# Optimization experiments

Measured on AMD Instinct MI355X. Metric: run time of the kernel, lower is better.

The kernel has to match this reference:

```python
import jax, jax.numpy as jnp
import numpy as np
from jax import lax

E, H, TOPK = 32, 512, 4
B, S = 2, 1024

def setup_inputs() -> dict:
    key = jax.random.key(0)
    ks = jax.random.split(key, 5)
    scale = 0.05
    return {
        "x": jax.random.normal(ks[0], (B, S, H), dtype=jnp.float32),
        "gate_w": jax.random.normal(ks[1], (E, H), dtype=jnp.float32) * scale,
        "w_gate": jax.random.normal(ks[2], (E, 2 * H, H), dtype=jnp.float32) * scale,
        "w_up": jax.random.normal(ks[3], (E, 2 * H, H), dtype=jnp.float32) * scale,
        "w_down": jax.random.normal(ks[4], (E, H, 2 * H), dtype=jnp.float32) * scale,
        "top_k": TOPK,
    }

def reference(x, gate_w, w_gate, w_up, w_down, top_k):
    b, s, h = x.shape
    n = b * s
    e = gate_w.shape[0]
    xf = x.reshape(n, h)                                   # [N,H]
    logits = xf @ gate_w.T                                 # [N,E]
    probs = jax.nn.softmax(logits, axis=-1)
    w, sel = lax.top_k(probs, top_k)                       # [N,K]
    w = w / jnp.sum(w, axis=-1, keepdims=True)
    # per-(token,expert) combine weight; zero for unselected experts
    comb = jnp.zeros((n, e), dtype=x.dtype).at[
        jnp.arange(n)[:, None], sel].add(w)                # [N,E]

    def body(acc, ws):
        wg, wu, wd, ce = ws                                # [2H,H],[2H,H],[H,2H],[N]
        hidden = jax.nn.silu(xf @ wg.T) * (xf @ wu.T)      # [N,2H]
        out = hidden @ wd.T                                # [N,H]
        return acc + out * ce[:, None], None

    acc0 = jnp.zeros_like(xf)
    acc, _ = lax.scan(body, acc0, (w_gate, w_up, w_down, comb.T))
    return acc.reshape(b, s, h)
```

## Files before the change

### kernel.cpp

```cpp
#include <hip/hip_runtime.h>
#include <hip/hip_bf16.h>
#include <math.h>

#define NE 32
#define H 512
#define H2 1024
#define NTOK 2048
#define CAP 2048
#define BM 64
#define MAXT64 160
#define TSTRIDE 144

typedef __attribute__((ext_vector_type(8))) short bf16x8;
typedef __attribute__((ext_vector_type(4))) float f32x4;
typedef unsigned int uint;
typedef unsigned short ushort;

__device__ __forceinline__ uint bf16r(float f) {
    uint u = __float_as_uint(f);
    return (u + 0x7FFFu + ((u >> 16) & 1u)) >> 16;
}
__device__ __forceinline__ uint pack_bf16(float a, float b) {
    return bf16r(a) | (bf16r(b) << 16);
}
__device__ __forceinline__ float bf16f(ushort u) {
    return __uint_as_float(((uint)u) << 16);
}

__device__ __forceinline__ void dma16(const void* g, void* l) {
    __builtin_amdgcn_global_load_lds(
        (const __attribute__((address_space(1))) uint*)g,
        (__attribute__((address_space(3))) uint*)l, 16, 0, 0);
}

__global__ __launch_bounds__(256) void prep_kernel(
    const float* __restrict__ x, const float* __restrict__ gate_w,
    int* __restrict__ cnt, int* __restrict__ listTok, int* __restrict__ listPair,
    float* __restrict__ listW, ushort* __restrict__ xbf,
    const float* __restrict__ wg, const float* __restrict__ wu,
    const float* __restrict__ wd,
    ushort* __restrict__ wgb, ushort* __restrict__ wub, ushort* __restrict__ wdb)
{
    const int b = blockIdx.x;
    if (b >= 512) {
        const int b2 = b - 512;
        const float* src = (b2 < 8192) ? wg : (b2 < 16384) ? wu : wd;
        ushort*     dst  = (b2 < 8192) ? wgb : (b2 < 16384) ? wub : wdb;
        const size_t base = (size_t)(b2 & 8191) * 2048 + (size_t)threadIdx.x * 8;
        const float4* s = (const float4*)(src + base);
        float4 x0 = s[0], x1 = s[1];
        uint4 v;
        v.x = pack_bf16(x0.x, x0.y); v.y = pack_bf16(x0.z, x0.w);
        v.z = pack_bf16(x1.x, x1.y); v.w = pack_bf16(x1.z, x1.w);
        *(uint4*)(dst + base) = v;
        return;
    }

    const int wave = threadIdx.x >> 6;
    const int lane = threadIdx.x & 63;
    const int t = b * 4 + wave;
    const int e = lane & 31;
    const int half = lane >> 5;

    const float4* xr = (const float4*)(x + (size_t)t * H + half * 256);
    const float4* gr = (const float4*)(gate_w + (size_t)e * H + half * 256);
    float acc = 0.f;
#pragma unroll 8
    for (int i = 0; i < 64; ++i) {
        float4 a = xr[i], g = gr[i];
        acc += a.x * g.x + a.y * g.y + a.z * g.z + a.w * g.w;
    }
    acc += __shfl_xor(acc, 32);

    float mx = acc;
#pragma unroll
    for (int m = 16; m >= 1; m >>= 1) mx = fmaxf(mx, __shfl_xor(mx, m));
    float p = __expf(acc - mx);
    float s = p;
#pragma unroll
    for (int m = 16; m >= 1; m >>= 1) s += __shfl_xor(s, m);
    float prob = p / s;

    int selk[4]; float wk[4]; float sum4 = 0.f;
#pragma unroll
    for (int k = 0; k < 4; ++k) {
        float v = prob; int idx = e;
#pragma unroll
        for (int m = 16; m >= 1; m >>= 1) {
            float v2 = __shfl_xor(v, m);
            int   i2 = __shfl_xor(idx, m);
            if (v2 > v || (v2 == v && i2 < idx)) { v = v2; idx = i2; }
        }
        selk[k] = idx; wk[k] = v; sum4 += v;
        if (e == idx) prob = -1.f;
    }

    if (lane == 0) {
#pragma unroll
        for (int k = 0; k < 4; ++k) {
            int ex = selk[k];
            int pos = atomicAdd(&cnt[ex], 1);
            listTok [ex * CAP + pos] = t;
            listPair[ex * CAP + pos] = t * 4 + k;
            listW   [ex * CAP + pos] = wk[k] / sum4;
        }
    }

    const float4* xrow4 = (const float4*)(x + (size_t)t * H);
    float4 a0 = xrow4[lane * 2];
    float4 a1 = xrow4[lane * 2 + 1];
    uint4 o;
    o.x = pack_bf16(a0.x, a0.y); o.y = pack_bf16(a0.z, a0.w);
    o.z = pack_bf16(a1.x, a1.y); o.w = pack_bf16(a1.z, a1.w);
    ((uint4*)(xbf + (size_t)t * H))[lane] = o;
}

__global__ void sched_kernel(const int* __restrict__ cnt,
                             int* __restrict__ ntiles, int* __restrict__ desc)
{
    const int lane = threadIdx.x;
    int t = 0;
    if (lane < NE) t = (cnt[lane] + 63) >> 6;
    int pre = t;
#pragma unroll
    for (int m = 1; m < 64; m <<= 1) {
        int v = __shfl_up(pre, m);
        if (lane >= m) pre += v;
    }
    const int off = pre - t;
    if (lane < NE)
        for (int i = 0; i < t; ++i) desc[off + i] = (lane << 16) | i;
    if (lane == 63) *ntiles = pre;
}

template<bool WB>
__global__ __launch_bounds__(256, 4) void moe_gemm1(
    const void* __restrict__ wgate_, const void* __restrict__ wup_,
    const ushort* __restrict__ xbf, const int* __restrict__ cnt,
    const int* __restrict__ listTok, const int* __restrict__ listPair,
    const float* __restrict__ listW, ushort* __restrict__ hidden,
    const int* __restrict__ ntiles, const int* __restrict__ desc)
{
    const int item = blockIdx.x;
    if (item >= (*ntiles) * 8) return;
    const int d  = desc[item >> 3];
    const int ch = item & 7;
    const int e  = d >> 16;
    const int mt = d & 0xffff;
    const int count = cnt[e];
    const int m0 = mt * BM;

    __shared__ ushort smem[2 * 128 * 64];
    ushort* Gs = smem;
    ushort* Us = smem + 128 * 64;

    const int tid  = threadIdx.x;
    const int lane = tid & 63;
    const int w    = tid >> 6;
    const int l15  = lane & 15;
    const int quad = lane >> 4;

    const int arow = m0 + w * 16 + l15;
    const int atok = (arow < count) ? listTok[e * CAP + arow] : 0;
    const char* aptr = (const char*)(xbf + (size_t)atok * H);

    const int rr = lane >> 3;
    const int p  = lane & 7;
    const char* gsrc = nullptr; const char* usrc = nullptr;
    const int sr = tid >> 1;
    const int sh = tid & 1;
    const float* gF = nullptr; const float* uF = nullptr;
    if (WB) {
        const ushort* wgp = (const ushort*)wgate_;
        const ushort* wup = (const ushort*)wup_;
        const size_t rowi = (size_t)e * H2 + (size_t)(ch * 128 + w * 32 + rr);
        gsrc = (const char*)(wgp + rowi * H) + ((p ^ rr) << 4);
        usrc = (const char*)(wup + rowi * H) + ((p ^ rr) << 4);
    } else {
        gF = (const float*)wgate_ + ((size_t)e * H2 + (size_t)(ch * 128 + sr)) * H;
        uF = (const float*)wup_   + ((size_t)e * H2 + (size_t)(ch * 128 + sr)) * H;
    }

    f32x4 accg[8], accu[8];
    const f32x4 fz = {0.f, 0.f, 0.f, 0.f};
#pragma unroll
    for (int ni = 0; ni < 8; ++ni) { accg[ni] = fz; accu[ni] = fz; }

    uint4 a0 = *(const uint4*)(aptr + quad * 16);
    uint4 a1 = *(const uint4*)(aptr + 64 + quad * 16);

    for (int it = 0; it < 8; ++it) {
        __syncthreads();
        if (WB) {
#pragma unroll
            for (int i = 0; i < 4; ++i) {
                dma16(gsrc + i * (8 * H * 2), (char*)Gs + w * 4096 + i * 1024);
                dma16(usrc + i * (8 * H * 2), (char*)Us + w * 4096 + i * 1024);
            }
        } else {
#pragma unroll
            for (int i = 0; i < 4; ++i) {
                const int pslot = sh * 4 + i;
                const int pc = pslot ^ (sr & 7);
                const float4* s1 = (const float4*)(gF + it * 64 + pc * 8);
                float4 g0 = s1[0], g1 = s1[1];
                uint4 v;
                v.x = pack_bf16(g0.x, g0.y); v.y = pack_bf16(g0.z, g0.w);
                v.z = pack_bf16(g1.x, g1.y); v.w = pack_bf16(g1.z, g1.w);
                ((uint4*)Gs)[sr * 8 + pslot] = v;
                const float4* s2 = (const float4*)(uF + it * 64 + pc * 8);
                float4 u0 = s2[0], u1 = s2[1];
                uint4 q;
                q.x = pack_bf16(u0.x, u0.y); q.y = pack_bf16(u0.z, u0.w);
                q.z = pack_bf16(u1.x, u1.y); q.w = pack_bf16(u1.z, u1.w);
                ((uint4*)Us)[sr * 8 + pslot] = q;
            }
        }
        const int itn = (it < 7) ? it + 1 : 7;
        uint4 an0 = *(const uint4*)(aptr + itn * 128 + quad * 16);
        uint4 an1 = *(const uint4*)(aptr + itn * 128 + 64 + quad * 16);
        __syncthreads();

#pragma unroll
        for (int ks = 0; ks < 2; ++ks) {
            bf16x8 af = ks ? *(bf16x8*)&a1 : *(bf16x8*)&a0;
#pragma unroll
            for (int ni = 0; ni < 8; ++ni) {
                const int n = ni * 16 + l15;
                const int slot = n * 8 + ((ks * 4 + quad) ^ (n & 7));
                bf16x8 bg = ((const bf16x8*)Gs)[slot];
                bf16x8 bu = ((const bf16x8*)Us)[slot];
                accg[ni] = __builtin_amdgcn_mfma_f32_16x16x32_bf16(af, bg, accg[ni], 0, 0, 0);
                accu[ni] = __builtin_amdgcn_mfma_f32_16x16x32_bf16(af, bu, accu[ni], 0, 0, 0);
            }
        }
        a0 = an0; a1 = an1;
        if (WB) { gsrc += 128; usrc += 128; }
    }

    __syncthreads();
    ushort* T = smem;
#pragma unroll
    for (int r = 0; r < 4; ++r) {
        const int row = w * 16 + quad * 4 + r;
        const int slot2 = m0 + row;
        const float wgt = (slot2 < count) ? listW[e * CAP + slot2] : 0.f;
#pragma unroll
        for (int ni = 0; ni < 8; ++ni) {
            float gv = accg[ni][r], uv = accu[ni][r];
            float hv = (gv / (1.f + __expf(-gv))) * uv * wgt;
            T[row * TSTRIDE + ni * 16 + l15] = (ushort)bf16r(hv);
        }
    }
    __syncthreads();
    {
        const int row = tid >> 2;
        const int qp  = tid & 3;
        const int slot2 = m0 + row;
        if (slot2 < count) {
            const int pr = listPair[e * CAP + slot2];
            uint4* dst = (uint4*)(hidden + (size_t)pr * H2 + ch * 128) + qp * 4;
            const uint4* src = (const uint4*)(T + row * TSTRIDE) + qp * 4;
#pragma unroll
            for (int i = 0; i < 4; ++i) dst[i] = src[i];
        }
    }
}

template<bool WB>
__global__ __launch_bounds__(256, 4) void moe_gemm2(
    const void* __restrict__ wdown_, const ushort* __restrict__ hidden,
    const int* __restrict__ cnt, const int* __restrict__ listPair,
    ushort* __restrict__ pairOut,
    const int* __restrict__ ntiles, const int* __restrict__ desc)
{
    const int item = blockIdx.x;
    if (item >= (*ntiles) * 8) return;
    const int d   = desc[item >> 3];
    const int ks2 = (item >> 2) & 1;
    const int ch  = item & 3;
    const int e   = d >> 16;
    const int mt  = d & 0xffff;
    const int count = cnt[e];
    const int m0 = mt * BM;

    __shared__ ushort smem[9216];
    ushort* Bs = smem;

    const int tid  = threadIdx.x;
    const int lane = tid & 63;
    const int w    = tid >> 6;
    const int l15  = lane & 15;
    const int quad = lane >> 4;

    const int arow = m0 + w * 16 + l15;
    const int apr  = (arow < count) ? listPair[e * CAP + arow] : 0;
    const char* aptr = (const char*)(hidden + (size_t)apr * H2 + ks2 * 512);

    const int rr = lane >> 3;
    const int p  = lane & 7;
    const char* bsrc = nullptr;
    const int sr = tid >> 1;
    const int sh = tid & 1;
    const float* bF = nullptr;
    if (WB) {
        const ushort* wdp = (const ushort*)wdown_;
        const size_t rowi = (size_t)e * H + (size_t)(ch * 128 + w * 32 + rr);
        bsrc = (const char*)(wdp + rowi * H2 + ks2 * 512) + ((p ^ rr) << 4);
    } else {
        bF = (const float*)wdown_ + ((size_t)e * H + (size_t)(ch * 128 + sr)) * H2 + ks2 * 512;
    }

    f32x4 acc[8];
    const f32x4 fz = {0.f, 0.f, 0.f, 0.f};
#pragma unroll
    for (int ni = 0; ni < 8; ++ni) acc[ni] = fz;

    uint4 a0 = *(const uint4*)(aptr + quad * 16);
    uint4 a1 = *(const uint4*)(aptr + 64 + quad * 16);

    for (int it = 0; it < 8; ++it) {
        __syncthreads();
        if (WB) {
#pragma unroll
            for (int i = 0; i < 4; ++i)
                dma16(bsrc + i * (8 * H2 * 2), (char*)Bs + w * 4096 + i * 1024);
        } else {
#pragma unroll
            for (int i = 0; i < 4; ++i) {
                const int pslot = sh * 4 + i;
                const int pc = pslot ^ (sr & 7);
                const float4* s1 = (const float4*)(bF + it * 64 + pc * 8);
                float4 b0 = s1[0], b1 = s1[1];
                uint4 v;
                v.x = pack_bf16(b0.x, b0.y); v.y = pack_bf16(b0.z, b0.w);
                v.z = pack_bf16(b1.x, b1.y); v.w = pack_bf16(b1.z, b1.w);
                ((uint4*)Bs)[sr * 8 + pslot] = v;
            }
        }
        const int itn = (it < 7) ? it + 1 : 7;
        uint4 an0 = *(const uint4*)(aptr + itn * 128 + quad * 16);
        uint4 an1 = *(const uint4*)(aptr + itn * 128 + 64 + quad * 16);
        __syncthreads();

#pragma unroll
        for (int ks = 0; ks < 2; ++ks) {
            bf16x8 af = ks ? *(bf16x8*)&a1 : *(bf16x8*)&a0;
#pragma unroll
            for (int ni = 0; ni < 8; ++ni) {
                const int n = ni * 16 + l15;
                const int slot = n * 8 + ((ks * 4 + quad) ^ (n & 7));
                bf16x8 bb = ((const bf16x8*)Bs)[slot];
                acc[ni] = __builtin_amdgcn_mfma_f32_16x16x32_bf16(af, bb, acc[ni], 0, 0, 0);
            }
        }
        a0 = an0; a1 = an1;
        if (WB) bsrc += 128;
    }

    __syncthreads();
    ushort* T = smem;
#pragma unroll
    for (int r = 0; r < 4; ++r) {
        const int row = w * 16 + quad * 4 + r;
#pragma unroll
        for (int ni = 0; ni < 8; ++ni)
            T[row * TSTRIDE + ni * 16 + l15] = (ushort)bf16r(acc[ni][r]);
    }
    __syncthreads();
    {
        const int row = tid >> 2;
        const int qp  = tid & 3;
        const int slot2 = m0 + row;
        if (slot2 < count) {
            const int pr = listPair[e * CAP + slot2];
            uint4* dst = (uint4*)(pairOut + ((size_t)(ks2 << 13) + pr) * H + ch * 128) + qp * 4;
            const uint4* src = (const uint4*)(T + row * TSTRIDE) + qp * 4;
#pragma unroll
            for (int i = 0; i < 4; ++i) dst[i] = src[i];
        }
    }
}

__global__ __launch_bounds__(256) void combine_kernel(
    const ushort* __restrict__ pairOut, float* __restrict__ out)
{
    const int tok = blockIdx.x * 4 + (threadIdx.x >> 6);
    const int c   = (threadIdx.x & 63) * 8;
    float s[8];
#pragma unroll
    for (int i = 0; i < 8; ++i) s[i] = 0.f;
#pragma unroll
    for (int j = 0; j < 8; ++j) {
        const int row = ((j >> 2) << 13) + tok * 4 + (j & 3);
        uint4 v = *(const uint4*)(pairOut + (size_t)row * H + c);
        const ushort* u = (const ushort*)&v;
#pragma unroll
        for (int i = 0; i < 8; ++i) s[i] += bf16f(u[i]);
    }
    float4* o = (float4*)(out + (size_t)tok * H + c);
    o[0] = make_float4(s[0], s[1], s[2], s[3]);
    o[1] = make_float4(s[4], s[5], s[6], s[7]);
}

extern "C" void kernel_launch(void* const* d_in, const int* in_sizes, int n_in,
                              void* d_out, int out_size, void* d_ws, size_t ws_size,
                              hipStream_t stream)
{
    (void)in_sizes; (void)n_in; (void)out_size;
    const float* x      = (const float*)d_in[0];
    const float* gate_w = (const float*)d_in[1];
    const float* w_gate = (const float*)d_in[2];
    const float* w_up   = (const float*)d_in[3];
    const float* w_down = (const float*)d_in[4];

    char* ws = (char*)d_ws;
    int* cnt    = (int*)ws;
    int* ntiles = (int*)(ws + 128);
    int* desc   = (int*)(ws + 256);

    size_t off = 1024;
    int*    listTok  = (int*)(ws + off);   off += (size_t)NE * CAP * 4;
    int*    listPair = (int*)(ws + off);   off += (size_t)NE * CAP * 4;
    float*  listW    = (float*)(ws + off); off += (size_t)NE * CAP * 4;
    ushort* xbf      = (ushort*)(ws + off); off += (size_t)NTOK * H * 2;
    ushort* hidden   = (ushort*)(ws + off); off += (size_t)NTOK * 4 * H2 * 2;
    ushort* pairOut  = (ushort*)(ws + off); off += (size_t)2 * NTOK * 4 * H * 2;
    ushort* wgb = (ushort*)(ws + off); off += (size_t)NE * H2 * H * 2;
    ushort* wub = (ushort*)(ws + off); off += (size_t)NE * H2 * H * 2;
    ushort* wdb = (ushort*)(ws + off); off += (size_t)NE * H * H2 * 2;
    const size_t need_full = off;

    const bool full = (ws_size >= need_full);

    hipMemsetAsync(ws, 0, 256, stream);

    if (full) {
        prep_kernel<<<512 + 3 * 8192, 256, 0, stream>>>(
            x, gate_w, cnt, listTok, listPair, listW, xbf,
            w_gate, w_up, w_down, wgb, wub, wdb);
        sched_kernel<<<1, 64, 0, stream>>>(cnt, ntiles, desc);
        moe_gemm1<true><<<MAXT64 * 8, 256, 0, stream>>>(
            (const void*)wgb, (const void*)wub, xbf, cnt, listTok, listPair,
            listW, hidden, ntiles, desc);
        moe_gemm2<true><<<MAXT64 * 8, 256, 0, stream>>>(
            (const void*)wdb, hidden, cnt, listPair, pairOut, ntiles, desc);
    } else {
        prep_kernel<<<512, 256, 0, stream>>>(
            x, gate_w, cnt, listTok, listPair, listW, xbf,
            w_gate, w_up, w_down, nullptr, nullptr, nullptr);
        sched_kernel<<<1, 64, 0, stream>>>(cnt, ntiles, desc);
        moe_gemm1<false><<<MAXT64 * 8, 256, 0, stream>>>(
            (const void*)w_gate, (const void*)w_up, xbf, cnt, listTok, listPair,
            listW, hidden, ntiles, desc);
        moe_gemm2<false><<<MAXT64 * 8, 256, 0, stream>>>(
            (const void*)w_down, hidden, cnt, listPair, pairOut, ntiles, desc);
    }
    combine_kernel<<<NTOK / 4, 256, 0, stream>>>(pairOut, (float*)d_out);
}
```

Before: 331.9 us.

## Drop separate bf16 weight pre-conversion; convert fp32 weights inline in GEMM tiles

Removes the pass that converted every expert weight to bf16 in workspace before the GEMMs. The fp32 weights are now read and packed to bf16 directly while filling the LDS tiles. The swizzle moves from the global read address to the LDS write slot, so global reads become contiguous. This avoids a full read-plus-write pass over about 200MB of weights, but the GEMMs now read fp32 (twice the bytes) and lose the async global-to-LDS DMA path.

Measured after the change: 394.0 us. 18.7% more time.

```diff
diff --git a/kernel.cpp b/kernel.cpp
--- a/kernel.cpp
+++ b/kernel.cpp
@@ -27,35 +27,12 @@
     return __uint_as_float(((uint)u) << 16);
 }
 
-__device__ __forceinline__ void dma16(const void* g, void* l) {
-    __builtin_amdgcn_global_load_lds(
-        (const __attribute__((address_space(1))) uint*)g,
-        (__attribute__((address_space(3))) uint*)l, 16, 0, 0);
-}
-
 __global__ __launch_bounds__(256) void prep_kernel(
     const float* __restrict__ x, const float* __restrict__ gate_w,
     int* __restrict__ cnt, int* __restrict__ listTok, int* __restrict__ listPair,
-    float* __restrict__ listW, ushort* __restrict__ xbf,
-    const float* __restrict__ wg, const float* __restrict__ wu,
-    const float* __restrict__ wd,
-    ushort* __restrict__ wgb, ushort* __restrict__ wub, ushort* __restrict__ wdb)
+    float* __restrict__ listW, ushort* __restrict__ xbf)
 {
     const int b = blockIdx.x;
-    if (b >= 512) {
-        const int b2 = b - 512;
-        const float* src = (b2 < 8192) ? wg : (b2 < 16384) ? wu : wd;
-        ushort*     dst  = (b2 < 8192) ? wgb : (b2 < 16384) ? wub : wdb;
-        const size_t base = (size_t)(b2 & 8191) * 2048 + (size_t)threadIdx.x * 8;
-        const float4* s = (const float4*)(src + base);
-        float4 x0 = s[0], x1 = s[1];
-        uint4 v;
-        v.x = pack_bf16(x0.x, x0.y); v.y = pack_bf16(x0.z, x0.w);
-        v.z = pack_bf16(x1.x, x1.y); v.w = pack_bf16(x1.z, x1.w);
-        *(uint4*)(dst + base) = v;
-        return;
-    }
-
     const int wave = threadIdx.x >> 6;
     const int lane = threadIdx.x & 63;
     const int t = b * 4 + wave;
@@ -133,9 +110,8 @@
     if (lane == 63) *ntiles = pre;
 }
 
-template<bool WB>
 __global__ __launch_bounds__(256, 4) void moe_gemm1(
-    const void* __restrict__ wgate_, const void* __restrict__ wup_,
+    const float* __restrict__ wgate_, const float* __restrict__ wup_,
     const ushort* __restrict__ xbf, const int* __restrict__ cnt,
     const int* __restrict__ listTok, const int* __restrict__ listPair,
     const float* __restrict__ listW, ushort* __restrict__ hidden,
@@ -164,22 +140,10 @@
     const int atok = (arow < count) ? listTok[e * CAP + arow] : 0;
     const char* aptr = (const char*)(xbf + (size_t)atok * H);
 
-    const int rr = lane >> 3;
-    const int p  = lane & 7;
-    const char* gsrc = nullptr; const char* usrc = nullptr;
     const int sr = tid >> 1;
     const int sh = tid & 1;
-    const float* gF = nullptr; const float* uF = nullptr;
-    if (WB) {
-        const ushort* wgp = (const ushort*)wgate_;
-        const ushort* wup = (const ushort*)wup_;
-        const size_t rowi = (size_t)e * H2 + (size_t)(ch * 128 + w * 32 + rr);
-        gsrc = (const char*)(wgp + rowi * H) + ((p ^ rr) << 4);
-        usrc = (const char*)(wup + rowi * H) + ((p ^ rr) << 4);
-    } else {
-        gF = (const float*)wgate_ + ((size_t)e * H2 + (size_t)(ch * 128 + sr)) * H;
-        uF = (const float*)wup_   + ((size_t)e * H2 + (size_t)(ch * 128 + sr)) * H;
-    }
+    const float* gF = wgate_ + ((size_t)e * H2 + (size_t)(ch * 128 + sr)) * H;
+    const float* uF = wup_   + ((size_t)e * H2 + (size_t)(ch * 128 + sr)) * H;
 
     f32x4 accg[8], accu[8];
     const f32x4 fz = {0.f, 0.f, 0.f, 0.f};
@@ -191,30 +155,22 @@
 
     for (int it = 0; it < 8; ++it) {
         __syncthreads();
-        if (WB) {
-#pragma unroll
-            for (int i = 0; i < 4; ++i) {
-                dma16(gsrc + i * (8 * H * 2), (char*)Gs + w * 4096 + i * 1024);
-                dma16(usrc + i * (8 * H * 2), (char*)Us + w * 4096 + i * 1024);
-            }
-        } else {
-#pragma unroll
-            for (int i = 0; i < 4; ++i) {
-                const int pslot = sh * 4 + i;
-                const int pc = pslot ^ (sr & 7);
-                const float4* s1 = (const float4*)(gF + it * 64 + pc * 8);
-                float4 g0 = s1[0], g1 = s1[1];
-                uint4 v;
-                v.x = pack_bf16(g0.x, g0.y); v.y = pack_bf16(g0.z, g0.w);
-                v.z = pack_bf16(g1.x, g1.y); v.w = pack_bf16(g1.z, g1.w);
-                ((uint4*)Gs)[sr * 8 + pslot] = v;
-                const float4* s2 = (const float4*)(uF + it * 64 + pc * 8);
-                float4 u0 = s2[0], u1 = s2[1];
-                uint4 q;
-                q.x = pack_bf16(u0.x, u0.y); q.y = pack_bf16(u0.z, u0.w);
-                q.z = pack_bf16(u1.x, u1.y); q.w = pack_bf16(u1.z, u1.w);
-                ((uint4*)Us)[sr * 8 + pslot] = q;
-            }
+#pragma unroll
+        for (int i = 0; i < 4; ++i) {
+            const int pslot = sh * 4 + i;
+            const int pc = pslot ^ (sr & 7);
+            const float4* s1 = (const float4*)(gF + it * 64 + pslot * 8);
+            float4 g0 = s1[0], g1 = s1[1];
+            uint4 v;
+            v.x = pack_bf16(g0.x, g0.y); v.y = pack_bf16(g0.z, g0.w);
+            v.z = pack_bf16(g1.x, g1.y); v.w = pack_bf16(g1.z, g1.w);
+            ((uint4*)Gs)[sr * 8 + pc] = v;
+            const float4* s2 = (const float4*)(uF + it * 64 + pslot * 8);
+            float4 u0 = s2[0], u1 = s2[1];
+            uint4 q;
+            q.x = pack_bf16(u0.x, u0.y); q.y = pack_bf16(u0.z, u0.w);
+            q.z = pack_bf16(u1.x, u1.y); q.w = pack_bf16(u1.z, u1.w);
+            ((uint4*)Us)[sr * 8 + pc] = q;
         }
         const int itn = (it < 7) ? it + 1 : 7;
         uint4 an0 = *(const uint4*)(aptr + itn * 128 + quad * 16);
@@ -235,7 +191,6 @@
             }
         }
         a0 = an0; a1 = an1;
-        if (WB) { gsrc += 128; usrc += 128; }
     }
 
     __syncthreads();
@@ -267,9 +222,8 @@
     }
 }
 
-template<bool WB>
 __global__ __launch_bounds__(256, 4) void moe_gemm2(
-    const void* __restrict__ wdown_, const ushort* __restrict__ hidden,
+    const float* __restrict__ wdown_, const ushort* __restrict__ hidden,
     const int* __restrict__ cnt, const int* __restrict__ listPair,
     ushort* __restrict__ pairOut,
     const int* __restrict__ ntiles, const int* __restrict__ desc)
@@ -297,19 +251,9 @@
     const int apr  = (arow < count) ? listPair[e * CAP + arow] : 0;
     const char* aptr = (const char*)(hidden + (size_t)apr * H2 + ks2 * 512);
 
-    const int rr = lane >> 3;
-    const int p  = lane & 7;
-    const char* bsrc = nullptr;
     const int sr = tid >> 1;
     const int sh = tid & 1;
-    const float* bF = nullptr;
-    if (WB) {
-        const ushort* wdp = (const ushort*)wdown_;
-        const size_t rowi = (size_t)e * H + (size_t)(ch * 128 + w * 32 + rr);
-        bsrc = (const char*)(wdp + rowi * H2 + ks2 * 512) + ((p ^ rr) << 4);
-    } else {
-        bF = (const float*)wdown_ + ((size_t)e * H + (size_t)(ch * 128 + sr)) * H2 + ks2 * 512;
-    }
+    const float* bF = wdown_ + ((size_t)e * H + (size_t)(ch * 128 + sr)) * H2 + ks2 * 512;
 
     f32x4 acc[8];
     const f32x4 fz = {0.f, 0.f, 0.f, 0.f};
@@ -321,22 +265,16 @@
 
     for (int it = 0; it < 8; ++it) {
         __syncthreads();
-        if (WB) {
-#pragma unroll
-            for (int i = 0; i < 4; ++i)
-                dma16(bsrc + i * (8 * H2 * 2), (char*)Bs + w * 4096 + i * 1024);
-        } else {
-#pragma unroll
-            for (int i = 0; i < 4; ++i) {
-                const int pslot = sh * 4 + i;
-                const int pc = pslot ^ (sr & 7);
-                const float4* s1 = (const float4*)(bF + it * 64 + pc * 8);
-                float4 b0 = s1[0], b1 = s1[1];
-                uint4 v;
-                v.x = pack_bf16(b0.x, b0.y); v.y = pack_bf16(b0.z, b0.w);
-                v.z = pack_bf16(b1.x, b1.y); v.w = pack_bf16(b1.z, b1.w);
-                ((uint4*)Bs)[sr * 8 + pslot] = v;
-            }
+#pragma unroll
+        for (int i = 0; i < 4; ++i) {
+            const int pslot = sh * 4 + i;
+            const int pc = pslot ^ (sr & 7);
+            const float4* s1 = (const float4*)(bF + it * 64 + pslot * 8);
+            float4 b0 = s1[0], b1 = s1[1];
+            uint4 v;
+            v.x = pack_bf16(b0.x, b0.y); v.y = pack_bf16(b0.z, b0.w);
+            v.z = pack_bf16(b1.x, b1.y); v.w = pack_bf16(b1.z, b1.w);
+            ((uint4*)Bs)[sr * 8 + pc] = v;
         }
         const int itn = (it < 7) ? it + 1 : 7;
         uint4 an0 = *(const uint4*)(aptr + itn * 128 + quad * 16);
@@ -355,7 +293,6 @@
             }
         }
         a0 = an0; a1 = an1;
-        if (WB) bsrc += 128;
     }
 
     __syncthreads();
@@ -407,7 +344,7 @@
                               void* d_out, int out_size, void* d_ws, size_t ws_size,
                               hipStream_t stream)
 {
-    (void)in_sizes; (void)n_in; (void)out_size;
+    (void)in_sizes; (void)n_in; (void)out_size; (void)ws_size;
     const float* x      = (const float*)d_in[0];
     const float* gate_w = (const float*)d_in[1];
     const float* w_gate = (const float*)d_in[2];
@@ -426,35 +363,16 @@
     ushort* xbf      = (ushort*)(ws + off); off += (size_t)NTOK * H * 2;
     ushort* hidden   = (ushort*)(ws + off); off += (size_t)NTOK * 4 * H2 * 2;
     ushort* pairOut  = (ushort*)(ws + off); off += (size_t)2 * NTOK * 4 * H * 2;
-    ushort* wgb = (ushort*)(ws + off); off += (size_t)NE * H2 * H * 2;
-    ushort* wub = (ushort*)(ws + off); off += (size_t)NE * H2 * H * 2;
-    ushort* wdb = (ushort*)(ws + off); off += (size_t)NE * H * H2 * 2;
-    const size_t need_full = off;
-
-    const bool full = (ws_size >= need_full);
 
     hipMemsetAsync(ws, 0, 256, stream);
 
-    if (full) {
-        prep_kernel<<<512 + 3 * 8192, 256, 0, stream>>>(
-            x, gate_w, cnt, listTok, listPair, listW, xbf,
-            w_gate, w_up, w_down, wgb, wub, wdb);
-        sched_kernel<<<1, 64, 0, stream>>>(cnt, ntiles, desc);
-        moe_gemm1<true><<<MAXT64 * 8, 256, 0, stream>>>(
-            (const void*)wgb, (const void*)wub, xbf, cnt, listTok, listPair,
-            listW, hidden, ntiles, desc);
-        moe_gemm2<true><<<MAXT64 * 8, 256, 0, stream>>>(
-            (const void*)wdb, hidden, cnt, listPair, pairOut, ntiles, desc);
-    } else {
-        prep_kernel<<<512, 256, 0, stream>>>(
-            x, gate_w, cnt, listTok, listPair, listW, xbf,
-            w_gate, w_up, w_down, nullptr, nullptr, nullptr);
-        sched_kernel<<<1, 64, 0, stream>>>(cnt, ntiles, desc);
-        moe_gemm1<false><<<MAXT64 * 8, 256, 0, stream>>>(
-            (const void*)w_gate, (const void*)w_up, xbf, cnt, listTok, listPair,
-            listW, hidden, ntiles, desc);
-        moe_gemm2<false><<<MAXT64 * 8, 256, 0, stream>>>(
-            (const void*)w_down, hidden, cnt, listPair, pairOut, ntiles, desc);
-    }
+    prep_kernel<<<512, 256, 0, stream>>>(
+        x, gate_w, cnt, listTok, listPair, listW, xbf);
+    sched_kernel<<<1, 64, 0, stream>>>(cnt, ntiles, desc);
+    moe_gemm1<<<MAXT64 * 8, 256, 0, stream>>>(
+        w_gate, w_up, xbf, cnt, listTok, listPair,
+        listW, hidden, ntiles, desc);
+    moe_gemm2<<<MAXT64 * 8, 256, 0, stream>>>(
+        w_down, hidden, cnt, listPair, pairOut, ntiles, desc);
     combine_kernel<<<NTOK / 4, 256, 0, stream>>>(pairOut, (float*)d_out);
 }
```
